# Kernel tuning notes

Hardware: AMD Instinct MI355X
Metric: run time of the kernel (lower is better)

Reference implementation:

```python
import jax, jax.numpy as jnp
import numpy as np

B, V, D, E, F, H, HD = 16, 1024, 16, 64, 16, 128, 64
GRAPH_LAYERS, FLOW_ITERS, DUAL_ITERS = 2, 10, 10
STEP, MOM, BIG = 0.01, 0.9, 1e9


def _build_graph():
    # circulant graph: node v's d-th out-neighbor is v + offs[d] (mod V); offsets paired (o, -o)
    offs = np.array([1, -1, 2, -2, 3, -3, 4, -4, 5, -5, 6, -6, 7, -7, 8, -8], dtype=np.int32)
    v = np.arange(V, dtype=np.int32)[:, None]
    d = np.broadcast_to(np.arange(D, dtype=np.int32)[None, :], (V, D))
    adj = ((v + offs[None, :]) % V).astype(np.int32)
    inv_adj = ((v - offs[None, :]) % V).astype(np.int32)
    in_idx = np.stack([inv_adj, d], axis=-1)    # d-th incoming edge of v == out-edge (inv_adj[v,d], slot d)
    rev_idx = np.stack([adj, d], axis=-1)       # out-edge (v,d) is the d-th incoming edge of adj[v,d]
    opp_idx = np.stack([adj, d ^ 1], axis=-1)   # opposite edge (w->v) is slot d^1 at w (paired offsets)
    bt = lambda x: jnp.asarray(np.broadcast_to(x[None], (B,) + x.shape).copy())
    return bt(adj), bt(inv_adj), bt(in_idx), bt(rev_idx), bt(opp_idx)


def setup_inputs() -> dict:
    key = jax.random.key(0)
    ks = jax.random.split(key, 16)
    adj_lst, inv_adj_lst, in_indices, rev_indices, opp_indices = _build_graph()
    rn = lambda k, shape, scale=1.0: jax.random.normal(k, shape, dtype=jnp.float32) * scale
    s = lambda fan: 1.0 / float(np.sqrt(fan))
    return {
        'demands': rn(ks[0], (B, V, 1)),
        'node_features': rn(ks[1], (B, V, F)),
        'edge_lengths': jax.random.uniform(ks[2], (B, V, D), dtype=jnp.float32),
        'norm_edge_lengths': jax.random.uniform(ks[3], (B, V, D), dtype=jnp.float32),
        'node_emb': rn(ks[4], (V, E)),
        'W_enc': rn(ks[5], (E + F, H), s(E + F)), 'b_enc': jnp.zeros((H,), jnp.float32),
        'W_gat': rn(ks[6], (H, H), s(H)), 'b_gat': jnp.zeros((H,), jnp.float32),
        'a_gat': rn(ks[7], (H,), s(H)),
        'W_gru_x': rn(ks[8], (H, 3 * H), s(H)), 'W_gru_h': rn(ks[9], (H, 3 * H), s(H)),
        'b_gru': jnp.zeros((3 * H,), jnp.float32),
        'W_dec1': rn(ks[10], (2 * H, HD), s(2 * H)), 'b_dec1': jnp.zeros((HD,), jnp.float32),
        'W_dec2': rn(ks[11], (HD, 1), s(HD)), 'b_dec2': jnp.zeros((1,), jnp.float32),
        'W_dual1': rn(ks[12], (H, HD), s(H)), 'b_dual1': jnp.zeros((HD,), jnp.float32),
        'W_dual2': rn(ks[13], (HD, 1), s(HD)), 'b_dual2': jnp.zeros((1,), jnp.float32),
        'adj_lst': adj_lst, 'inv_adj_lst': inv_adj_lst,
        'in_indices': in_indices, 'rev_indices': rev_indices, 'opp_indices': opp_indices,
        'num_nodes': jnp.full((B,), V, dtype=jnp.int32),
    }


def _gather_nodes(values, idx, valid):
    # masked_gather with set_zero=True: values (B,V,H), idx (B,V,D) -> (B,V,D,H)
    bb = jnp.arange(values.shape[0])[:, None, None]
    g = values[bb, jnp.clip(idx, 0, values.shape[1] - 1)]
    return g * valid[..., None]


def _gather_edges(x, idx):
    # gather_nd into a (B,V,D,...) tensor; idx (B,V,D,2) = (node, slot), batch implicit
    bb = jnp.arange(x.shape[0])[:, None, None]
    return x[bb, idx[..., 0], idx[..., 1]]


def _sparsemax(z):
    n = z.shape[-1]
    zs = jnp.sort(z, axis=-1)[..., ::-1]
    k = jnp.arange(1, n + 1, dtype=z.dtype)
    zc = jnp.cumsum(zs, axis=-1)
    support = (1.0 + k * zs) > zc
    kz = jnp.sum(support, axis=-1, keepdims=True)
    tau = (jnp.take_along_axis(zc, kz - 1, axis=-1) - 1.0) / kz.astype(z.dtype)
    return jnp.maximum(z - tau, 0.0)


def _forward(demands, node_features, edge_lengths, norm_edge_lengths, node_emb, W_enc, b_enc,
             W_gat, b_gat, a_gat, W_gru_x, W_gru_h, b_gru, W_dec1, b_dec1, W_dec2, b_dec2,
             W_dual1, b_dual1, W_dual2, b_dual2,
             adj_lst, inv_adj_lst, in_indices, rev_indices, opp_indices, num_nodes):
    f32 = jnp.float32
    # embedding lookup with max_norm=1
    nrm = jnp.linalg.norm(node_emb, axis=-1, keepdims=True)
    emb = node_emb / jnp.maximum(nrm, 1.0)
    emb_b = jnp.broadcast_to(emb[None], (demands.shape[0], V, E))
    node_enc = jnp.concatenate([emb_b, node_features], axis=-1) @ W_enc + b_enc   # (B,V,H)
    mask = (adj_lst == num_nodes[:, None, None]).astype(f32)                       # 1 = padded slot
    valid = 1.0 - mask
    initial = _gather_nodes(node_enc, adj_lst, valid)                              # (B,V,D,H)
    h = initial
    for _ in range(GRAPH_LAYERS):
        # DirectionalGAT: per-edge transform, masked attention over slots, directional regather
        t = jnp.tanh(h @ W_gat + b_gat)                                            # (B,V,D,H)
        logits = jnp.einsum('bvdh,h->bvd', t, a_gat) - BIG * mask
        attn = jax.nn.softmax(logits, axis=-1)
        node_msg = jnp.einsum('bvd,bvdh->bvh', attn, t)                            # (B,V,H)
        msg = _gather_nodes(node_msg, adj_lst, valid)
        x = jnp.tanh(msg + initial)
        # GRU cell, shared weights over all edge states
        gx = x @ W_gru_x + b_gru
        gh = h @ W_gru_h
        z = jax.nn.sigmoid(gx[..., :H] + gh[..., :H])
        r = jax.nn.sigmoid(gx[..., H:2 * H] + gh[..., H:2 * H])
        cand = jnp.tanh(gx[..., 2 * H:] + r * gh[..., 2 * H:])
        h = z * h + (1.0 - z) * cand
    # decoder over (encoding, encoding + opposite-edge encoding)
    comb = h + _gather_edges(h, opp_indices)
    dec_in = jnp.concatenate([h, comb], axis=-1)
    nw = (jnp.tanh(dec_in @ W_dec1 + b_dec1) @ W_dec2 + b_dec2)[..., 0]            # (B,V,D)
    # destination attention: normalize over incoming edges, map back to outgoing layout
    inv_mask = (inv_adj_lst == num_nodes[:, None, None]).astype(f32)
    in_w = _gather_edges(nw, in_indices)
    dest_attn = jax.nn.softmax(in_w - BIG * inv_mask, axis=-1)
    nw = _gather_edges(dest_attn, rev_indices)
    pred = nw - BIG * mask
    normalized = _sparsemax(pred) * valid
    # iterative proportional min-cost-flow solver
    def mcf_step(flow, _):
        inflow = jnp.sum(_gather_edges(flow, in_indices), axis=-1, keepdims=True)  # (B,V,1)
        return normalized * jax.nn.relu(inflow - demands), None
    flow, _ = jax.lax.scan(mcf_step, jnp.zeros_like(normalized), None, length=FLOW_ITERS)
    flow_cost = jnp.sum(flow * flow, axis=(1, 2))                                  # square cost fn
    # dual variables + dual flow (projected momentum gradient descent)
    node_states = jnp.sum(h, axis=2)                                               # (B,V,H)
    dual_vars = jax.nn.relu(jnp.tanh(node_states @ W_dual1 + b_dual1) @ W_dual2 + b_dual2)  # (B,V,1)
    dual = mask * dual_vars
    dual_tr = _gather_nodes(dual_vars, adj_lst, valid)[..., 0]
    dual_diff = dual_tr - dual                                                     # (B,V,D)
    def dual_step(carry, _):
        f, vel = carry
        grad = 2.0 * f + dual_diff                                                 # d/df [f^2 + dual_diff*f]
        vel = MOM * vel - STEP * grad
        f = jax.nn.relu(f + vel)
        return (f, vel), None
    (dual_flows, _), _ = jax.lax.scan(dual_step, (jnp.zeros_like(dual_diff), jnp.zeros_like(dual_diff)), None, length=DUAL_ITERS)
    dual_flows = dual_flows * valid
    dual_demand = jnp.sum(dual_vars * demands, axis=(1, 2))
    dual_cost = jnp.sum(dual_flows * dual_flows + dual_diff * dual_flows, axis=(1, 2)) - dual_demand
    return flow_cost - dual_cost                                                   # (B,) primal-dual gap loss


def reference(demands, node_features, edge_lengths, norm_edge_lengths, node_emb, W_enc, b_enc,
              W_gat, b_gat, a_gat, W_gru_x, W_gru_h, b_gru, W_dec1, b_dec1, W_dec2, b_dec2,
              W_dual1, b_dual1, W_dual2, b_dual2,
              adj_lst, inv_adj_lst, in_indices, rev_indices, opp_indices, num_nodes):
    return _forward(demands, node_features, edge_lengths, norm_edge_lengths, node_emb, W_enc, b_enc,
                    W_gat, b_gat, a_gat, W_gru_x, W_gru_h, b_gru, W_dec1, b_dec1, W_dec2, b_dec2,
                    W_dual1, b_dual1, W_dual2, b_dual2,
                    adj_lst, inv_adj_lst, in_indices, rev_indices, opp_indices, num_nodes)
```

## Files before the change

### kernel.cpp

```cpp
#include <hip/hip_runtime.h>
#include <hip/hip_bf16.h>

#define B 16
#define V 1024
#define D 16
#define E 64
#define F 16
#define H 128
#define HD 64
#define BV (B*V)
#define BVD (B*V*D)

#define OFF_HNB      0
#define OFF_NORM     (OFF_HNB + BV*H/2)
#define OFF_DV       (OFF_NORM + BVD)
#define OFF_WT       (OFF_DV + BV)
#define OFF_WTG      (OFF_WT + 65536)
#define OFF_WPQ      (OFF_WTG + 8192)
#define OFF_WU1T     (OFF_WPQ + 8192)
#define OFF_WENCT    (OFF_WU1T + 4096)

typedef __attribute__((ext_vector_type(8))) short bf16x8;
typedef __attribute__((ext_vector_type(4))) float f32x4;

__device__ __forceinline__ short f2bf(float f){
  __hip_bfloat16 b = __float2bfloat16(f);
  return *reinterpret_cast<short*>(&b);
}
__device__ __forceinline__ float bf2f(short s){
  __hip_bfloat16 b; *reinterpret_cast<short*>(&b) = s;
  return __bfloat162float(b);
}
__device__ __forceinline__ float frcp(float x){ return __builtin_amdgcn_rcpf(x); }
__device__ __forceinline__ float fsig(float x){ return frcp(1.f + __expf(-x)); }
__device__ __forceinline__ float ftanh(float x){
  float e = __expf(-2.f*fabsf(x));
  float r = (1.f - e)*frcp(1.f + e);
  return copysignf(r, x);
}

__global__ __launch_bounds__(256) void k_pre(const float* __restrict__ Wx, const float* __restrict__ Wh,
    const float* __restrict__ Wg, const float* __restrict__ W1, const float* __restrict__ Wu1,
    const float* __restrict__ Wenc,
    short* __restrict__ Wt, short* __restrict__ Wgt, short* __restrict__ Wpq,
    short* __restrict__ Wu1t, short* __restrict__ Wenct, float* __restrict__ outz){
  int bid = blockIdx.x, tid = threadIdx.x;
  if (bid == 0 && tid < 16) outz[tid] = 0.f;
  if (bid < 512){
    int n = bid, k = tid;
    int g = n >> 7, j = n & 127;
    float v;
    if (g == 0)      v = (k < 128) ? Wx[k*384 + j]       : Wh[(k-128)*384 + j];
    else if (g == 1) v = (k < 128) ? Wx[k*384 + 128 + j] : Wh[(k-128)*384 + 128 + j];
    else if (g == 2) v = (k < 128) ? Wx[k*384 + 256 + j] : 0.f;
    else             v = (k < 128) ? 0.f                 : Wh[(k-128)*384 + 256 + j];
    Wt[n*256 + k] = f2bf(v);
    return;
  }
  if (bid < 576){
    int idx = (bid-512)*256 + tid;
    int n = idx >> 7, k = idx & 127;
    Wgt[n*128 + k] = f2bf(Wg[k*128 + n]);
    return;
  }
  if (bid < 608){
    int idx = (bid-576)*256 + tid;
    int n = idx >> 7, k = idx & 127;
    float wb = W1[(k+128)*HD + n];
    float wa = W1[k*HD + n];
    Wpq[n*128 + k]      = f2bf(wa + wb);
    Wpq[(64+n)*128 + k] = f2bf(wb);
    return;
  }
  if (bid < 640){
    int idx = (bid-608)*256 + tid;
    int n = idx >> 7, k = idx & 127;
    Wu1t[n*128 + k] = f2bf(Wu1[k*HD + n]);
    return;
  }
  {
    int nn = (bid-640)*2 + (tid >> 7);
    int kk = tid & 127;
    if (kk < 96) Wenct[nn*96 + kk] = f2bf(kk < 80 ? Wenc[kk*128 + nn] : 0.f);
  }
}

__global__ __launch_bounds__(512,4) void k_mega(const float* __restrict__ emb, const float* __restrict__ nf,
    const short* __restrict__ Wenct, const float* __restrict__ benc, const int* __restrict__ adj,
    const short* __restrict__ Wgt, const float* __restrict__ bg, const float* __restrict__ ag,
    const short* __restrict__ Wt, const float* __restrict__ bgru, short* __restrict__ hout){
  __shared__ short NE[64][136];
  __shared__ short T[64][136];
  __shared__ short H1[48][136];
  __shared__ short X[48][136];
  __shared__ float Lp[8][64];
  __shared__ float Ls[64];
  __shared__ float nrmv[64];
  short (*As)[136] = T;

  int tid = threadIdx.x;
  int blk = blockIdx.x;
  int b = blk >> 5;
  int n0 = (blk & 31) << 5;
  int w = tid >> 6, lane = tid & 63;
  int l15 = lane & 15, quad = lane >> 4;

  if (tid < 64){
    int v = (n0 - 16 + tid) & 1023;
    const float4* e4 = reinterpret_cast<const float4*>(&emb[v*E]);
    float ss = 0.f;
    #pragma unroll
    for (int q=0;q<16;q++){ float4 x = e4[q]; ss += x.x*x.x + x.y*x.y + x.z*x.z + x.w*x.w; }
    nrmv[tid] = frcp(fmaxf(sqrtf(ss), 1.f));
  }
  __syncthreads();
  for (int e=tid; e<64*16; e+=512){
    int r = e >> 4, q = e & 15;
    int v = (n0 - 16 + r) & 1023;
    float4 x = reinterpret_cast<const float4*>(&emb[v*E])[q];
    float iv = nrmv[r];
    short4 s; s.x=f2bf(x.x*iv); s.y=f2bf(x.y*iv); s.z=f2bf(x.z*iv); s.w=f2bf(x.w*iv);
    *reinterpret_cast<short4*>(&As[r][q*4]) = s;
  }
  for (int e=tid; e<64*4; e+=512){
    int r = e >> 2, q = e & 3;
    int m = (b<<10) + ((n0 - 16 + r) & 1023);
    float4 x = reinterpret_cast<const float4*>(&nf[(long)m*F])[q];
    short4 s; s.x=f2bf(x.x); s.y=f2bf(x.y); s.z=f2bf(x.z); s.w=f2bf(x.w);
    *reinterpret_cast<short4*>(&As[r][64 + q*4]) = s;
    short4 z; z.x=0; z.y=0; z.z=0; z.w=0;
    *reinterpret_cast<short4*>(&As[r][80 + q*4]) = z;
  }
  __syncthreads();
  {
    f32x4 acc[4];
    #pragma unroll
    for (int mt=0;mt<4;mt++) acc[mt] = (f32x4){0.f,0.f,0.f,0.f};
    #pragma unroll
    for (int kc=0;kc<3;kc++){
      int k0 = kc*32;
      bf16x8 bfr = *reinterpret_cast<const bf16x8*>(&Wenct[(16*w + l15)*96 + k0 + quad*8]);
      #pragma unroll
      for (int mt=0;mt<4;mt++){
        bf16x8 a = *reinterpret_cast<const bf16x8*>(&As[16*mt + l15][k0 + quad*8]);
        acc[mt] = __builtin_amdgcn_mfma_f32_16x16x32_bf16(a, bfr, acc[mt], 0,0,0);
      }
    }
    int c = 16*w + l15;
    float bb = benc[c];
    #pragma unroll
    for (int mt=0;mt<4;mt++)
      #pragma unroll
      for (int reg=0;reg<4;reg++)
        NE[16*mt + quad*4 + reg][c] = f2bf(acc[mt][reg] + bb);
  }
  __syncthreads();
  {
    f32x4 acc[4];
    #pragma unroll
    for (int mt=0;mt<4;mt++) acc[mt] = (f32x4){0.f,0.f,0.f,0.f};
    #pragma unroll
    for (int kc=0;kc<4;kc++){
      int k0 = kc*32;
      bf16x8 bfr = *reinterpret_cast<const bf16x8*>(&Wgt[(16*w + l15)*128 + k0 + quad*8]);
      #pragma unroll
      for (int mt=0;mt<4;mt++){
        bf16x8 a = *reinterpret_cast<const bf16x8*>(&NE[16*mt + l15][k0 + quad*8]);
        acc[mt] = __builtin_amdgcn_mfma_f32_16x16x32_bf16(a, bfr, acc[mt], 0,0,0);
      }
    }
    int c = 16*w + l15;
    float bgc = bg[c], agc = ag[c];
    float lp[4][4];
    #pragma unroll
    for (int mt=0;mt<4;mt++)
      #pragma unroll
      for (int reg=0;reg<4;reg++){
        float t = ftanh(acc[mt][reg] + bgc);
        T[16*mt + quad*4 + reg][c] = f2bf(t);
        lp[mt][reg] = t * agc;
      }
    #pragma unroll
    for (int mt=0;mt<4;mt++)
      #pragma unroll
      for (int reg=0;reg<4;reg++){
        lp[mt][reg] += __shfl_xor(lp[mt][reg], 1);
        lp[mt][reg] += __shfl_xor(lp[mt][reg], 2);
        lp[mt][reg] += __shfl_xor(lp[mt][reg], 4);
        lp[mt][reg] += __shfl_xor(lp[mt][reg], 8);
      }
    if (l15 == 0){
      #pragma unroll
      for (int mt=0;mt<4;mt++)
        #pragma unroll
        for (int reg=0;reg<4;reg++)
          Lp[w][16*mt + quad*4 + reg] = lp[mt][reg];
    }
  }
  __syncthreads();
  if (tid < 64){
    float s = 0.f;
    #pragma unroll
    for (int i=0;i<8;i++) s += Lp[i][tid];
    Ls[tid] = s;
  }
  __syncthreads();
  if (tid < 192){
    int vl = tid >> 2, seg = tid & 3;
    int wg = (b<<10) + ((n0 - 8 + vl) & 1023);
    int li[16]; float at[16];
    float m = -1e30f;
    #pragma unroll
    for (int d=0; d<16; d++){
      int a = adj[wg*16 + d];
      li[d] = (a - n0 + 16) & 1023;
      m = fmaxf(m, Ls[li[d]]);
    }
    float s = 0.f;
    #pragma unroll
    for (int d=0; d<16; d++){ at[d] = __expf(Ls[li[d]] - m); s += at[d]; }
    float inv = frcp(s);
    #pragma unroll
    for (int d=0; d<16; d++) at[d] *= inv;
    #pragma unroll
    for (int c8=0; c8<4; c8++){
      int c = seg*32 + c8*8;
      float acc8[8] = {0,0,0,0,0,0,0,0};
      #pragma unroll 4
      for (int d=0; d<16; d++){
        bf16x8 tv = *reinterpret_cast<const bf16x8*>(&T[li[d]][c]);
        float a = at[d];
        #pragma unroll
        for (int q=0;q<8;q++) acc8[q] += a * bf2f(tv[q]);
      }
      bf16x8 nv = *reinterpret_cast<const bf16x8*>(&NE[vl + 8][c]);
      bf16x8 xv;
      #pragma unroll
      for (int q=0;q<8;q++) xv[q] = f2bf(ftanh(acc8[q] + bf2f(nv[q])));
      *reinterpret_cast<bf16x8*>(&X[vl][c]) = xv;
    }
  }
  __syncthreads();
  {
    f32x4 acc[3][4];
    #pragma unroll
    for (int mt=0;mt<3;mt++)
      #pragma unroll
      for (int g=0;g<4;g++) acc[mt][g] = (f32x4){0.f,0.f,0.f,0.f};
    for (int k8=0;k8<8;k8++){
      int k0 = k8*32;
      int gg = (k8 < 4) ? 2 : 3;
      int ncol = 16*w + l15;
      int koff = k0 + quad*8;
      bf16x8 bz = *reinterpret_cast<const bf16x8*>(&Wt[(ncol      )*256 + koff]);
      bf16x8 br = *reinterpret_cast<const bf16x8*>(&Wt[(ncol + 128)*256 + koff]);
      bf16x8 bc = *reinterpret_cast<const bf16x8*>(&Wt[(ncol + gg*128)*256 + koff]);
      #pragma unroll
      for (int mt=0;mt<3;mt++){
        bf16x8 a;
        if (k8 < 4) a = *reinterpret_cast<const bf16x8*>(&X[16*mt + l15][k0 + quad*8]);
        else        a = *reinterpret_cast<const bf16x8*>(&NE[16*mt + l15 + 8][k0 - 128 + quad*8]);
        acc[mt][0]  = __builtin_amdgcn_mfma_f32_16x16x32_bf16(a, bz, acc[mt][0], 0,0,0);
        acc[mt][1]  = __builtin_amdgcn_mfma_f32_16x16x32_bf16(a, br, acc[mt][1], 0,0,0);
        acc[mt][gg] = __builtin_amdgcn_mfma_f32_16x16x32_bf16(a, bc, acc[mt][gg], 0,0,0);
      }
    }
    int j = 16*w + l15;
    float bjz = bgru[j], bjr = bgru[128 + j], bjc = bgru[256 + j];
    #pragma unroll
    for (int mt=0;mt<3;mt++){
      #pragma unroll
      for (int reg=0;reg<4;reg++){
        int rl = 16*mt + quad*4 + reg;
        float z = fsig(acc[mt][0][reg] + bjz);
        float r = fsig(acc[mt][1][reg] + bjr);
        float cand = ftanh(acc[mt][2][reg] + bjc + r*acc[mt][3][reg]);
        float ho = bf2f(NE[rl + 8][j]);
        H1[rl][j] = f2bf(z*ho + (1.f - z)*cand);
      }
    }
  }
  __syncthreads();
  {
    f32x4 acc[3];
    #pragma unroll
    for (int mt=0;mt<3;mt++) acc[mt] = (f32x4){0.f,0.f,0.f,0.f};
    #pragma unroll
    for (int kc=0;kc<4;kc++){
      int k0 = kc*32;
      bf16x8 bfr = *reinterpret_cast<const bf16x8*>(&Wgt[(16*w + l15)*128 + k0 + quad*8]);
      #pragma unroll
      for (int mt=0;mt<3;mt++){
        bf16x8 a = *reinterpret_cast<const bf16x8*>(&H1[16*mt + l15][k0 + quad*8]);
        acc[mt] = __builtin_amdgcn_mfma_f32_16x16x32_bf16(a, bfr, acc[mt], 0,0,0);
      }
    }
    int c = 16*w + l15;
    float bgc = bg[c], agc = ag[c];
    float lp[3][4];
    #pragma unroll
    for (int mt=0;mt<3;mt++)
      #pragma unroll
      for (int reg=0;reg<4;reg++){
        float t = ftanh(acc[mt][reg] + bgc);
        T[16*mt + quad*4 + reg][c] = f2bf(t);
        lp[mt][reg] = t * agc;
      }
    #pragma unroll
    for (int mt=0;mt<3;mt++)
      #pragma unroll
      for (int reg=0;reg<4;reg++){
        lp[mt][reg] += __shfl_xor(lp[mt][reg], 1);
        lp[mt][reg] += __shfl_xor(lp[mt][reg], 2);
        lp[mt][reg] += __shfl_xor(lp[mt][reg], 4);
        lp[mt][reg] += __shfl_xor(lp[mt][reg], 8);
      }
    if (l15 == 0){
      #pragma unroll
      for (int mt=0;mt<3;mt++)
        #pragma unroll
        for (int reg=0;reg<4;reg++)
          Lp[w][16*mt + quad*4 + reg] = lp[mt][reg];
    }
  }
  __syncthreads();
  if (tid < 48){
    float s = 0.f;
    #pragma unroll
    for (int i=0;i<8;i++) s += Lp[i][tid];
    Ls[tid] = s;
  }
  __syncthreads();
  if (tid < 128){
    int vl = tid >> 2, seg = tid & 3;
    int vg = (b<<10) + n0 + vl;
    int li[16]; float at[16];
    float m = -1e30f;
    #pragma unroll
    for (int d=0; d<16; d++){
      int a = adj[vg*16 + d];
      li[d] = (a - n0 + 8) & 1023;
      m = fmaxf(m, Ls[li[d]]);
    }
    float s = 0.f;
    #pragma unroll
    for (int d=0; d<16; d++){ at[d] = __expf(Ls[li[d]] - m); s += at[d]; }
    float inv = frcp(s);
    #pragma unroll
    for (int d=0; d<16; d++) at[d] *= inv;
    #pragma unroll
    for (int c8=0; c8<4; c8++){
      int c = seg*32 + c8*8;
      float acc8[8] = {0,0,0,0,0,0,0,0};
      #pragma unroll 4
      for (int d=0; d<16; d++){
        bf16x8 tv = *reinterpret_cast<const bf16x8*>(&T[li[d]][c]);
        float a = at[d];
        #pragma unroll
        for (int q=0;q<8;q++) acc8[q] += a * bf2f(tv[q]);
      }
      bf16x8 nv = *reinterpret_cast<const bf16x8*>(&NE[vl + 16][c]);
      bf16x8 xv;
      #pragma unroll
      for (int q=0;q<8;q++) xv[q] = f2bf(ftanh(acc8[q] + bf2f(nv[q])));
      *reinterpret_cast<bf16x8*>(&X[vl][c]) = xv;
    }
  }
  __syncthreads();
  {
    f32x4 acc[2][4];
    #pragma unroll
    for (int mt=0;mt<2;mt++)
      #pragma unroll
      for (int g=0;g<4;g++) acc[mt][g] = (f32x4){0.f,0.f,0.f,0.f};
    for (int k8=0;k8<8;k8++){
      int k0 = k8*32;
      int gg = (k8 < 4) ? 2 : 3;
      int ncol = 16*w + l15;
      int koff = k0 + quad*8;
      bf16x8 bz = *reinterpret_cast<const bf16x8*>(&Wt[(ncol      )*256 + koff]);
      bf16x8 br = *reinterpret_cast<const bf16x8*>(&Wt[(ncol + 128)*256 + koff]);
      bf16x8 bc = *reinterpret_cast<const bf16x8*>(&Wt[(ncol + gg*128)*256 + koff]);
      #pragma unroll
      for (int mt=0;mt<2;mt++){
        bf16x8 a;
        if (k8 < 4) a = *reinterpret_cast<const bf16x8*>(&X[16*mt + l15][k0 + quad*8]);
        else        a = *reinterpret_cast<const bf16x8*>(&H1[16*mt + l15 + 8][k0 - 128 + quad*8]);
        acc[mt][0]  = __builtin_amdgcn_mfma_f32_16x16x32_bf16(a, bz, acc[mt][0], 0,0,0);
        acc[mt][1]  = __builtin_amdgcn_mfma_f32_16x16x32_bf16(a, br, acc[mt][1], 0,0,0);
        acc[mt][gg] = __builtin_amdgcn_mfma_f32_16x16x32_bf16(a, bc, acc[mt][gg], 0,0,0);
      }
    }
    __syncthreads();
    int j = 16*w + l15;
    float bjz = bgru[j], bjr = bgru[128 + j], bjc = bgru[256 + j];
    #pragma unroll
    for (int mt=0;mt<2;mt++){
      #pragma unroll
      for (int reg=0;reg<4;reg++){
        int rl = 16*mt + quad*4 + reg;
        float z = fsig(acc[mt][0][reg] + bjz);
        float r = fsig(acc[mt][1][reg] + bjr);
        float cand = ftanh(acc[mt][2][reg] + bjc + r*acc[mt][3][reg]);
        float ho = bf2f(H1[rl + 8][j]);
        X[rl][j] = f2bf(z*ho + (1.f - z)*cand);
      }
    }
  }
  __syncthreads();
  for (int idx=tid; idx<32*16; idx+=512){
    int r = idx >> 4, c8 = idx & 15;
    *reinterpret_cast<bf16x8*>(&hout[(long)((b<<10) + n0 + r)*128 + c8*8]) =
        *reinterpret_cast<const bf16x8*>(&X[r][c8*8]);
  }
}

__global__ __launch_bounds__(512,2) void k_decdas(const short* __restrict__ hn, const int* __restrict__ adj,
    const int* __restrict__ invadj, const short* __restrict__ Wpq, const float* __restrict__ b1,
    const float* __restrict__ W2, const float* __restrict__ b2_,
    const short* __restrict__ Wu1t, const float* __restrict__ bu1, const float* __restrict__ Wu2,
    const float* __restrict__ bu2_, float* __restrict__ norm_, float* __restrict__ dv){
  __shared__ short Hs[112][136];
  __shared__ short PQb[112][132];
  __shared__ short NSs[64][136];
  __shared__ int adjL[64][16];
  __shared__ float dvp[64][4];
  __shared__ float b1s[64], w2s[64], bu1s[64], wu2s[64];
  int tid = threadIdx.x;
  int blk = blockIdx.x;
  int b = blk >> 4;
  int n0 = (blk & 15) << 6;
  if (tid < 64){ b1s[tid] = b1[tid]; w2s[tid] = W2[tid]; bu1s[tid] = bu1[tid]; wu2s[tid] = Wu2[tid]; }
  for (int idx=tid; idx<112*16; idx+=512){
    int r = idx >> 4, c8 = idx & 15;
    int g = (b << 10) + ((n0 - 24 + r) & 1023);
    *reinterpret_cast<bf16x8*>(&Hs[r][c8*8]) =
        *reinterpret_cast<const bf16x8*>(&hn[(long)g*128 + c8*8]);
  }
  for (int idx=tid; idx<1024; idx+=512){
    int r = idx >> 4, d = idx & 15;
    int a = adj[((b<<10) + n0 + r)*16 + d];
    adjL[r][d] = (a - n0 + 24) & 1023;
  }
  __syncthreads();
  int w = tid >> 6, lane = tid & 63;
  int l15 = lane & 15, quad = lane >> 4;
  {
    f32x4 acc[7];
    #pragma unroll
    for (int mt=0;mt<7;mt++) acc[mt] = (f32x4){0.f,0.f,0.f,0.f};
    #pragma unroll
    for (int kc=0;kc<4;kc++){
      int k0 = kc*32;
      bf16x8 bfr = *reinterpret_cast<const bf16x8*>(&Wpq[(16*w + l15)*128 + k0 + quad*8]);
      #pragma unroll
      for (int mt=0;mt<7;mt++){
        bf16x8 a = *reinterpret_cast<const bf16x8*>(&Hs[16*mt + l15][k0 + quad*8]);
        acc[mt] = __builtin_amdgcn_mfma_f32_16x16x32_bf16(a, bfr, acc[mt], 0,0,0);
      }
    }
    int c = 16*w + l15;
    #pragma unroll
    for (int mt=0;mt<7;mt++)
      #pragma unroll
      for (int reg=0;reg<4;reg++)
        PQb[16*mt + quad*4 + reg][c] = f2bf(acc[mt][reg]);
  }
  for (int idx=tid; idx<64*16; idx+=512){
    int r = idx >> 4, c8 = idx & 15;
    float acc8[8] = {0,0,0,0,0,0,0,0};
    #pragma unroll 4
    for (int d=0; d<16; d++){
      bf16x8 hv = *reinterpret_cast<const bf16x8*>(&Hs[adjL[r][d]][c8*8]);
      #pragma unroll
      for (int q=0;q<8;q++) acc8[q] += bf2f(hv[q]);
    }
    bf16x8 sv;
    #pragma unroll
    for (int q=0;q<8;q++) sv[q] = f2bf(acc8[q]);
    *reinterpret_cast<bf16x8*>(&NSs[r][c8*8]) = sv;
  }
  __syncthreads();
  if (w < 4){
    f32x4 acc[4];
    #pragma unroll
    for (int mt=0;mt<4;mt++) acc[mt] = (f32x4){0.f,0.f,0.f,0.f};
    #pragma unroll
    for (int kc=0;kc<4;kc++){
      int k0 = kc*32;
      bf16x8 bfr = *reinterpret_cast<const bf16x8*>(&Wu1t[(16*w + l15)*128 + k0 + quad*8]);
      #pragma unroll
      for (int mt=0;mt<4;mt++){
        bf16x8 a = *reinterpret_cast<const bf16x8*>(&NSs[16*mt + l15][k0 + quad*8]);
        acc[mt] = __builtin_amdgcn_mfma_f32_16x16x32_bf16(a, bfr, acc[mt], 0,0,0);
      }
    }
    int n = 16*w + l15;
    float bn = bu1s[n], wn = wu2s[n];
    #pragma unroll
    for (int mt=0;mt<4;mt++){
      #pragma unroll
      for (int reg=0;reg<4;reg++){
        float p = ftanh(acc[mt][reg] + bn) * wn;
        p += __shfl_xor(p, 1);
        p += __shfl_xor(p, 2);
        p += __shfl_xor(p, 4);
        p += __shfl_xor(p, 8);
        if (l15 == 0) dvp[16*mt + quad*4 + reg][w] = p;
      }
    }
  }
  __syncthreads();
  float* nws = reinterpret_cast<float*>(&Hs[0][0]);
  float b2v = b2_[0];
  for (int e = tid; e < 96*16; e += 512){
    int rr = e >> 4, d = e & 15;
    int wnode = (n0 + rr - 16) & 1023;
    int wg = (b<<10) + wnode;
    int a = adj[wg*16 + d];
    int al = (a - n0 + 24) & 1023;
    int wl = rr + 8;
    float p = 0.f;
    #pragma unroll 8
    for (int c=0;c<64;c++)
      p += ftanh(bf2f(PQb[al][c]) + bf2f(PQb[wl][64 + c]) + b1s[c]) * w2s[c];
    nws[rr*17 + d] = p + b2v;
  }
  __syncthreads();
  if (tid < 64){
    float val = dvp[tid][0]+dvp[tid][1]+dvp[tid][2]+dvp[tid][3];
    dv[(b<<10) + n0 + tid] = fmaxf(val + bu2_[0], 0.f);
  }
  float* datt = reinterpret_cast<float*>(&PQb[0][0]);
  if (tid < 80){
    int wnode = (n0 + tid - 8) & 1023;
    int wg = (b<<10) + wnode;
    float vals[16];
    float m = -1e30f;
    #pragma unroll
    for (int d=0; d<16; d++){
      int iv = invadj[wg*16 + d];
      int il = (iv - n0 + 16) & 1023;
      vals[d] = nws[il*17 + d];
      m = fmaxf(m, vals[d]);
    }
    float s = 0.f;
    #pragma unroll
    for (int d=0; d<16; d++){ vals[d] = __expf(vals[d]-m); s += vals[d]; }
    float inv = frcp(s);
    #pragma unroll
    for (int d=0; d<16; d++) datt[tid*17 + d] = vals[d]*inv;
  }
  __syncthreads();
  if (tid < 64){
    int vg = (b<<10) + n0 + tid;
    float z[16], s[16];
    #pragma unroll
    for (int d=0; d<16; d++){
      int al = adjL[tid][d] - 16;
      z[d] = datt[al*17 + d];
      s[d] = z[d];
    }
    #pragma unroll
    for (int k2 = 2; k2 <= 16; k2 <<= 1){
      #pragma unroll
      for (int jj = k2 >> 1; jj > 0; jj >>= 1){
        #pragma unroll
        for (int i = 0; i < 16; i++){
          int l = i ^ jj;
          if (l > i){
            bool up = ((i & k2) == 0);
            float a = s[i], bb = s[l];
            bool sw = up ? (a > bb) : (a < bb);
            if (sw){ s[i]=bb; s[l]=a; }
          }
        }
      }
    }
    float cs = 0.f, zcs = 0.f; int kz = 1;
    #pragma unroll
    for (int j=0;j<16;j++){
      float zj = s[15-j];
      cs += zj;
      if (1.f + (float)(j+1)*zj > cs){ kz = j+1; zcs = cs; }
    }
    float tau = (zcs - 1.f)/(float)kz;
    #pragma unroll
    for (int d=0; d<16; d++) norm_[(long)vg*16 + d] = fmaxf(z[d]-tau, 0.f);
  }
}

__global__ __launch_bounds__(256) void k_flowfin(const float* __restrict__ norm_,
    const float* __restrict__ dem, const int* __restrict__ invadj, const float* __restrict__ dv,
    float* __restrict__ out){
  __shared__ float nrmS[224*17];
  __shared__ float sbuf[2][224];
  __shared__ float red[4];
  int tid = threadIdx.x;
  int blk = blockIdx.x;
  int b = blk >> 4;
  int t0 = (blk & 15) << 6;
  for (int e=tid; e<224*4; e+=256){
    int r = e >> 2, q4 = e & 3;
    int v = (t0 - 80 + r) & 1023;
    float4 x = reinterpret_cast<const float4*>(&norm_[(long)((b<<10) + v)*16])[q4];
    nrmS[r*17 + q4*4+0] = x.x; nrmS[r*17 + q4*4+1] = x.y;
    nrmS[r*17 + q4*4+2] = x.z; nrmS[r*17 + q4*4+3] = x.w;
  }
  bool act = tid < 224;
  int r = tid;
  float dm = 0.f; int gv = 0;
  int ivl[16];
  if (act){
    int v = (t0 - 80 + r) & 1023;
    gv = (b<<10) + v;
    dm = dem[gv];
    #pragma unroll
    for (int d4=0; d4<4; d4++){
      int4 i4 = reinterpret_cast<const int4*>(&invadj[(long)gv*16])[d4];
      int t;
      t = (i4.x - t0 + 80) & 1023; ivl[d4*4+0] = t < 224 ? t : 223;
      t = (i4.y - t0 + 80) & 1023; ivl[d4*4+1] = t < 224 ? t : 223;
      t = (i4.z - t0 + 80) & 1023; ivl[d4*4+2] = t < 224 ? t : 223;
      t = (i4.w - t0 + 80) & 1023; ivl[d4*4+3] = t < 224 ? t : 223;
    }
    sbuf[0][r] = 0.f;
  }
  __syncthreads();
  float nrg[16];
  if (act){
    #pragma unroll
    for (int d=0; d<16; d++) nrg[d] = nrmS[ivl[d]*17 + d];
  }
  int p = 0;
  float s = 0.f;
  for (int it=0; it<10; it++){
    if (act){
      float inflow = 0.f;
      #pragma unroll
      for (int d=0; d<16; d++) inflow += nrg[d]*sbuf[p][ivl[d]];
      s = fmaxf(inflow - dm, 0.f);
      sbuf[1-p][r] = s;
    }
    p ^= 1;
    __syncthreads();
  }
  float partF = 0.f, partD = 0.f, partDD = 0.f;
  if (act && r >= 80 && r < 144){
    float nr2 = 0.f;
    #pragma unroll
    for (int d=0; d<16; d++){ float nv = nrmS[r*17 + d]; nr2 += nv*nv; }
    partF = nr2 * s * s;
    float dvv = dv[gv];
    float f = 0.f, vel = 0.f;
    #pragma unroll
    for (int it=0; it<10; it++){
      float g = 2.f*f + dvv;
      vel = 0.9f*vel - 0.01f*g;
      f = fmaxf(f + vel, 0.f);
    }
    partD = f*f + dvv*f;
    partDD = dvv * dm;
  }
  float val = partF - 16.f*partD + partDD;
  #pragma unroll
  for (int off=32; off>0; off>>=1) val += __shfl_down(val, off);
  if ((tid & 63) == 0) red[tid>>6] = val;
  __syncthreads();
  if (tid == 0) atomicAdd(&out[b], red[0]+red[1]+red[2]+red[3]);
}

extern "C" void kernel_launch(void* const* d_in, const int* in_sizes, int n_in,
                              void* d_out, int out_size, void* d_ws, size_t ws_size,
                              hipStream_t stream){
  (void)in_sizes; (void)n_in; (void)out_size; (void)ws_size;
  const float* demands = (const float*)d_in[0];
  const float* nf      = (const float*)d_in[1];
  const float* emb     = (const float*)d_in[4];
  const float* Wenc    = (const float*)d_in[5];
  const float* benc    = (const float*)d_in[6];
  const float* Wgat    = (const float*)d_in[7];
  const float* bgat    = (const float*)d_in[8];
  const float* agat    = (const float*)d_in[9];
  const float* Wgx     = (const float*)d_in[10];
  const float* Wgh     = (const float*)d_in[11];
  const float* bgru    = (const float*)d_in[12];
  const float* Wd1     = (const float*)d_in[13];
  const float* bd1     = (const float*)d_in[14];
  const float* Wd2     = (const float*)d_in[15];
  const float* bd2     = (const float*)d_in[16];
  const float* Wu1     = (const float*)d_in[17];
  const float* bu1     = (const float*)d_in[18];
  const float* Wu2     = (const float*)d_in[19];
  const float* bu2     = (const float*)d_in[20];
  const int* adj       = (const int*)d_in[21];
  const int* invadj    = (const int*)d_in[22];

  float* ws    = (float*)d_ws;
  short* hnB   = (short*)(ws + OFF_HNB);
  float* nrm   = ws + OFF_NORM;
  float* dv    = ws + OFF_DV;
  short* wt    = (short*)(ws + OFF_WT);
  short* wtg   = (short*)(ws + OFF_WTG);
  short* wpq   = (short*)(ws + OFF_WPQ);
  short* wu1t  = (short*)(ws + OFF_WU1T);
  short* wenct = (short*)(ws + OFF_WENCT);

  k_pre<<<704, 256, 0, stream>>>(Wgx, Wgh, Wgat, Wd1, Wu1, Wenc, wt, wtg, wpq, wu1t, wenct,
                                 (float*)d_out);
  k_mega<<<BV/32, 512, 0, stream>>>(emb, nf, wenct, benc, adj, wtg, bgat, agat, wt, bgru, hnB);
  k_decdas<<<BV/64, 512, 0, stream>>>(hnB, adj, invadj, wpq, bd1, Wd2, bd2,
                                      wu1t, bu1, Wu2, bu2, nrm, dv);
  k_flowfin<<<B*16, 256, 0, stream>>>(nrm, demands, invadj, dv, (float*)d_out);
}
```

Measured before the change: 194.4 us.

## Widen graph tiles to 64 nodes, GAT aggregation as dense MFMA, 1024-thread decoder

k_mega now processes 64 output nodes per block instead of 32, cutting the halo recomputation of the encoder/GAT/GRU layers relative to useful rows. The attention-weighted neighbor aggregation is rewritten as a dense banded attention matrix (A2) times a transposed T tile on MFMA instead of scalar gather-FMA loops. Adjacency is loaded once per thread and reused for both layers. k_decdas is relaunched with 1024 threads, splitting its MFMA and neighbor-sum work across more waves. The trade-off is more LDS per block, lower occupancy bounds, and extra zero-fill of the mostly sparse A2 matrix.

```diff
diff --git a/kernel.cpp b/kernel.cpp
--- a/kernel.cpp
+++ b/kernel.cpp
@@ -85,36 +85,54 @@
   }
 }
 
-__global__ __launch_bounds__(512,4) void k_mega(const float* __restrict__ emb, const float* __restrict__ nf,
+__global__ __launch_bounds__(512,2) void k_mega(const float* __restrict__ emb, const float* __restrict__ nf,
     const short* __restrict__ Wenct, const float* __restrict__ benc, const int* __restrict__ adj,
     const short* __restrict__ Wgt, const float* __restrict__ bg, const float* __restrict__ ag,
     const short* __restrict__ Wt, const float* __restrict__ bgru, short* __restrict__ hout){
-  __shared__ short NE[64][136];
-  __shared__ short T[64][136];
-  __shared__ short H1[48][136];
-  __shared__ short X[48][136];
-  __shared__ float Lp[8][64];
-  __shared__ float Ls[64];
-  __shared__ float nrmv[64];
-  short (*As)[136] = T;
+  __shared__ short NE[96][136];
+  __shared__ short Tt[128][104];
+  __shared__ short H1[80][136];
+  __shared__ short X[80][136];
+  __shared__ short A2[80][104];
+  __shared__ float Lp[8][96];
+  __shared__ float Ls[96];
+  __shared__ float nrmv[96];
+  short (*As)[104] = reinterpret_cast<short(*)[104]>(&H1[0][0]);
 
   int tid = threadIdx.x;
   int blk = blockIdx.x;
-  int b = blk >> 5;
-  int n0 = (blk & 31) << 5;
+  int b = blk >> 4;
+  int n0 = (blk & 15) << 6;
   int w = tid >> 6, lane = tid & 63;
   int l15 = lane & 15, quad = lane >> 4;
 
-  if (tid < 64){
-    int v = (n0 - 16 + tid) & 1023;
+  int li96[16];
+  if (tid < 80){
+    int wg = (b<<10) + ((n0 - 8 + tid) & 1023);
+    const int4* a4 = reinterpret_cast<const int4*>(&adj[(long)wg*16]);
+    #pragma unroll
+    for (int d4=0; d4<4; d4++){
+      int4 i4 = a4[d4];
+      li96[d4*4+0] = (i4.x - n0 + 16) & 1023;
+      li96[d4*4+1] = (i4.y - n0 + 16) & 1023;
+      li96[d4*4+2] = (i4.z - n0 + 16) & 1023;
+      li96[d4*4+3] = (i4.w - n0 + 16) & 1023;
+    }
+  }
+
+  if (tid < 384){
+    int r = tid >> 2, q = tid & 3;
+    int v = (n0 - 16 + r) & 1023;
     const float4* e4 = reinterpret_cast<const float4*>(&emb[v*E]);
     float ss = 0.f;
     #pragma unroll
-    for (int q=0;q<16;q++){ float4 x = e4[q]; ss += x.x*x.x + x.y*x.y + x.z*x.z + x.w*x.w; }
-    nrmv[tid] = frcp(fmaxf(sqrtf(ss), 1.f));
-  }
-  __syncthreads();
-  for (int e=tid; e<64*16; e+=512){
+    for (int qq=0;qq<4;qq++){ float4 x = e4[q*4+qq]; ss += x.x*x.x + x.y*x.y + x.z*x.z + x.w*x.w; }
+    ss += __shfl_xor(ss, 1);
+    ss += __shfl_xor(ss, 2);
+    if (q == 0) nrmv[r] = frcp(fmaxf(sqrtf(ss), 1.f));
+  }
+  __syncthreads();
+  for (int e=tid; e<96*16; e+=512){
     int r = e >> 4, q = e & 15;
     int v = (n0 - 16 + r) & 1023;
     float4 x = reinterpret_cast<const float4*>(&emb[v*E])[q];
@@ -122,7 +140,7 @@
     short4 s; s.x=f2bf(x.x*iv); s.y=f2bf(x.y*iv); s.z=f2bf(x.z*iv); s.w=f2bf(x.w*iv);
     *reinterpret_cast<short4*>(&As[r][q*4]) = s;
   }
-  for (int e=tid; e<64*4; e+=512){
+  for (int e=tid; e<96*4; e+=512){
     int r = e >> 2, q = e & 3;
     int m = (b<<10) + ((n0 - 16 + r) & 1023);
     float4 x = reinterpret_cast<const float4*>(&nf[(long)m*F])[q];
@@ -133,15 +151,15 @@
   }
   __syncthreads();
   {
-    f32x4 acc[4];
-    #pragma unroll
-    for (int mt=0;mt<4;mt++) acc[mt] = (f32x4){0.f,0.f,0.f,0.f};
+    f32x4 acc[6];
+    #pragma unroll
+    for (int mt=0;mt<6;mt++) acc[mt] = (f32x4){0.f,0.f,0.f,0.f};
     #pragma unroll
     for (int kc=0;kc<3;kc++){
       int k0 = kc*32;
       bf16x8 bfr = *reinterpret_cast<const bf16x8*>(&Wenct[(16*w + l15)*96 + k0 + quad*8]);
       #pragma unroll
-      for (int mt=0;mt<4;mt++){
+      for (int mt=0;mt<6;mt++){
         bf16x8 a = *reinterpret_cast<const bf16x8*>(&As[16*mt + l15][k0 + quad*8]);
         acc[mt] = __builtin_amdgcn_mfma_f32_16x16x32_bf16(a, bfr, acc[mt], 0,0,0);
       }
@@ -149,39 +167,42 @@
     int c = 16*w + l15;
     float bb = benc[c];
     #pragma unroll
-    for (int mt=0;mt<4;mt++)
+    for (int mt=0;mt<6;mt++)
       #pragma unroll
       for (int reg=0;reg<4;reg++)
         NE[16*mt + quad*4 + reg][c] = f2bf(acc[mt][reg] + bb);
   }
   __syncthreads();
   {
-    f32x4 acc[4];
-    #pragma unroll
-    for (int mt=0;mt<4;mt++) acc[mt] = (f32x4){0.f,0.f,0.f,0.f};
+    f32x4 acc[6];
+    #pragma unroll
+    for (int mt=0;mt<6;mt++) acc[mt] = (f32x4){0.f,0.f,0.f,0.f};
     #pragma unroll
     for (int kc=0;kc<4;kc++){
       int k0 = kc*32;
       bf16x8 bfr = *reinterpret_cast<const bf16x8*>(&Wgt[(16*w + l15)*128 + k0 + quad*8]);
       #pragma unroll
-      for (int mt=0;mt<4;mt++){
+      for (int mt=0;mt<6;mt++){
         bf16x8 a = *reinterpret_cast<const bf16x8*>(&NE[16*mt + l15][k0 + quad*8]);
         acc[mt] = __builtin_amdgcn_mfma_f32_16x16x32_bf16(a, bfr, acc[mt], 0,0,0);
       }
     }
     int c = 16*w + l15;
     float bgc = bg[c], agc = ag[c];
-    float lp[4][4];
-    #pragma unroll
-    for (int mt=0;mt<4;mt++)
+    float lp[6][4];
+    #pragma unroll
+    for (int mt=0;mt<6;mt++){
+      short4 tv;
       #pragma unroll
       for (int reg=0;reg<4;reg++){
         float t = ftanh(acc[mt][reg] + bgc);
-        T[16*mt + quad*4 + reg][c] = f2bf(t);
+        reinterpret_cast<short*>(&tv)[reg] = f2bf(t);
         lp[mt][reg] = t * agc;
       }
-    #pragma unroll
-    for (int mt=0;mt<4;mt++)
+      *reinterpret_cast<short4*>(&Tt[c][16*mt + quad*4]) = tv;
+    }
+    #pragma unroll
+    for (int mt=0;mt<6;mt++)
       #pragma unroll
       for (int reg=0;reg<4;reg++){
         lp[mt][reg] += __shfl_xor(lp[mt][reg], 1);
@@ -191,60 +212,70 @@
       }
     if (l15 == 0){
       #pragma unroll
-      for (int mt=0;mt<4;mt++)
+      for (int mt=0;mt<6;mt++)
         #pragma unroll
         for (int reg=0;reg<4;reg++)
           Lp[w][16*mt + quad*4 + reg] = lp[mt][reg];
     }
   }
   __syncthreads();
-  if (tid < 64){
+  if (tid < 96){
     float s = 0.f;
     #pragma unroll
     for (int i=0;i<8;i++) s += Lp[i][tid];
     Ls[tid] = s;
   }
-  __syncthreads();
-  if (tid < 192){
-    int vl = tid >> 2, seg = tid & 3;
-    int wg = (b<<10) + ((n0 - 8 + vl) & 1023);
-    int li[16]; float at[16];
+  {
+    bf16x8 z8;
+    #pragma unroll
+    for (int q=0;q<8;q++) z8[q] = 0;
+    for (int idx=tid; idx<960; idx+=512){
+      int r = idx/12, c8 = idx%12;
+      *reinterpret_cast<bf16x8*>(&A2[r][c8*8]) = z8;
+    }
+  }
+  __syncthreads();
+  if (tid < 80){
+    float at[16];
     float m = -1e30f;
     #pragma unroll
-    for (int d=0; d<16; d++){
-      int a = adj[wg*16 + d];
-      li[d] = (a - n0 + 16) & 1023;
-      m = fmaxf(m, Ls[li[d]]);
-    }
+    for (int d=0; d<16; d++) m = fmaxf(m, Ls[li96[d]]);
     float s = 0.f;
     #pragma unroll
-    for (int d=0; d<16; d++){ at[d] = __expf(Ls[li[d]] - m); s += at[d]; }
+    for (int d=0; d<16; d++){ at[d] = __expf(Ls[li96[d]] - m); s += at[d]; }
     float inv = frcp(s);
     #pragma unroll
-    for (int d=0; d<16; d++) at[d] *= inv;
-    #pragma unroll
-    for (int c8=0; c8<4; c8++){
-      int c = seg*32 + c8*8;
-      float acc8[8] = {0,0,0,0,0,0,0,0};
-      #pragma unroll 4
-      for (int d=0; d<16; d++){
-        bf16x8 tv = *reinterpret_cast<const bf16x8*>(&T[li[d]][c]);
-        float a = at[d];
-        #pragma unroll
-        for (int q=0;q<8;q++) acc8[q] += a * bf2f(tv[q]);
-      }
-      bf16x8 nv = *reinterpret_cast<const bf16x8*>(&NE[vl + 8][c]);
-      bf16x8 xv;
-      #pragma unroll
-      for (int q=0;q<8;q++) xv[q] = f2bf(ftanh(acc8[q] + bf2f(nv[q])));
-      *reinterpret_cast<bf16x8*>(&X[vl][c]) = xv;
-    }
-  }
-  __syncthreads();
-  {
-    f32x4 acc[3][4];
-    #pragma unroll
-    for (int mt=0;mt<3;mt++)
+    for (int d=0; d<16; d++) A2[tid][li96[d]] = f2bf(at[d]*inv);
+  }
+  __syncthreads();
+  {
+    f32x4 acc[5];
+    #pragma unroll
+    for (int mt=0;mt<5;mt++) acc[mt] = (f32x4){0.f,0.f,0.f,0.f};
+    #pragma unroll
+    for (int kc=0;kc<3;kc++){
+      int k0 = kc*32;
+      bf16x8 bfr = *reinterpret_cast<const bf16x8*>(&Tt[16*w + l15][k0 + quad*8]);
+      #pragma unroll
+      for (int mt=0;mt<5;mt++){
+        bf16x8 a = *reinterpret_cast<const bf16x8*>(&A2[16*mt + l15][k0 + quad*8]);
+        acc[mt] = __builtin_amdgcn_mfma_f32_16x16x32_bf16(a, bfr, acc[mt], 0,0,0);
+      }
+    }
+    int c = 16*w + l15;
+    #pragma unroll
+    for (int mt=0;mt<5;mt++)
+      #pragma unroll
+      for (int reg=0;reg<4;reg++){
+        int rl = 16*mt + quad*4 + reg;
+        X[rl][c] = f2bf(ftanh(acc[mt][reg] + bf2f(NE[rl + 8][c])));
+      }
+  }
+  __syncthreads();
+  {
+    f32x4 acc[5][4];
+    #pragma unroll
+    for (int mt=0;mt<5;mt++)
       #pragma unroll
       for (int g=0;g<4;g++) acc[mt][g] = (f32x4){0.f,0.f,0.f,0.f};
     for (int k8=0;k8<8;k8++){
@@ -256,7 +287,7 @@
       bf16x8 br = *reinterpret_cast<const bf16x8*>(&Wt[(ncol + 128)*256 + koff]);
       bf16x8 bc = *reinterpret_cast<const bf16x8*>(&Wt[(ncol + gg*128)*256 + koff]);
       #pragma unroll
-      for (int mt=0;mt<3;mt++){
+      for (int mt=0;mt<5;mt++){
         bf16x8 a;
         if (k8 < 4) a = *reinterpret_cast<const bf16x8*>(&X[16*mt + l15][k0 + quad*8]);
         else        a = *reinterpret_cast<const bf16x8*>(&NE[16*mt + l15 + 8][k0 - 128 + quad*8]);
@@ -268,7 +299,7 @@
     int j = 16*w + l15;
     float bjz = bgru[j], bjr = bgru[128 + j], bjc = bgru[256 + j];
     #pragma unroll
-    for (int mt=0;mt<3;mt++){
+    for (int mt=0;mt<5;mt++){
       #pragma unroll
       for (int reg=0;reg<4;reg++){
         int rl = 16*mt + quad*4 + reg;
@@ -282,32 +313,35 @@
   }
   __syncthreads();
   {
-    f32x4 acc[3];
-    #pragma unroll
-    for (int mt=0;mt<3;mt++) acc[mt] = (f32x4){0.f,0.f,0.f,0.f};
+    f32x4 acc[5];
+    #pragma unroll
+    for (int mt=0;mt<5;mt++) acc[mt] = (f32x4){0.f,0.f,0.f,0.f};
     #pragma unroll
     for (int kc=0;kc<4;kc++){
       int k0 = kc*32;
       bf16x8 bfr = *reinterpret_cast<const bf16x8*>(&Wgt[(16*w + l15)*128 + k0 + quad*8]);
       #pragma unroll
-      for (int mt=0;mt<3;mt++){
+      for (int mt=0;mt<5;mt++){
         bf16x8 a = *reinterpret_cast<const bf16x8*>(&H1[16*mt + l15][k0 + quad*8]);
         acc[mt] = __builtin_amdgcn_mfma_f32_16x16x32_bf16(a, bfr, acc[mt], 0,0,0);
       }
     }
     int c = 16*w + l15;
     float bgc = bg[c], agc = ag[c];
-    float lp[3][4];
-    #pragma unroll
-    for (int mt=0;mt<3;mt++)
+    float lp[5][4];
+    #pragma unroll
+    for (int mt=0;mt<5;mt++){
+      short4 tv;
       #pragma unroll
       for (int reg=0;reg<4;reg++){
         float t = ftanh(acc[mt][reg] + bgc);
-        T[16*mt + quad*4 + reg][c] = f2bf(t);
+        reinterpret_cast<short*>(&tv)[reg] = f2bf(t);
         lp[mt][reg] = t * agc;
       }
-    #pragma unroll
-    for (int mt=0;mt<3;mt++)
+      *reinterpret_cast<short4*>(&Tt[c][16*mt + quad*4]) = tv;
+    }
+    #pragma unroll
+    for (int mt=0;mt<5;mt++)
       #pragma unroll
       for (int reg=0;reg<4;reg++){
         lp[mt][reg] += __shfl_xor(lp[mt][reg], 1);
@@ -317,60 +351,71 @@
       }
     if (l15 == 0){
       #pragma unroll
-      for (int mt=0;mt<3;mt++)
+      for (int mt=0;mt<5;mt++)
         #pragma unroll
         for (int reg=0;reg<4;reg++)
           Lp[w][16*mt + quad*4 + reg] = lp[mt][reg];
     }
   }
   __syncthreads();
-  if (tid < 48){
+  if (tid < 80){
     float s = 0.f;
     #pragma unroll
     for (int i=0;i<8;i++) s += Lp[i][tid];
     Ls[tid] = s;
   }
-  __syncthreads();
-  if (tid < 128){
-    int vl = tid >> 2, seg = tid & 3;
-    int vg = (b<<10) + n0 + vl;
-    int li[16]; float at[16];
+  {
+    bf16x8 z8;
+    #pragma unroll
+    for (int q=0;q<8;q++) z8[q] = 0;
+    for (int idx=tid; idx<768; idx+=512){
+      int r = idx/12, c8 = idx%12;
+      *reinterpret_cast<bf16x8*>(&A2[r][c8*8]) = z8;
+    }
+  }
+  __syncthreads();
+  if (tid >= 8 && tid < 72){
+    int r5 = tid - 8;
+    float at[16];
     float m = -1e30f;
     #pragma unroll
-    for (int d=0; d<16; d++){
-      int a = adj[vg*16 + d];
-      li[d] = (a - n0 + 8) & 1023;
-      m = fmaxf(m, Ls[li[d]]);
-    }
+    for (int d=0; d<16; d++) m = fmaxf(m, Ls[li96[d] - 8]);
     float s = 0.f;
     #pragma unroll
-    for (int d=0; d<16; d++){ at[d] = __expf(Ls[li[d]] - m); s += at[d]; }
+    for (int d=0; d<16; d++){ at[d] = __expf(Ls[li96[d] - 8] - m); s += at[d]; }
     float inv = frcp(s);
     #pragma unroll
-    for (int d=0; d<16; d++) at[d] *= inv;
-    #pragma unroll
-    for (int c8=0; c8<4; c8++){
-      int c = seg*32 + c8*8;
-      float acc8[8] = {0,0,0,0,0,0,0,0};
-      #pragma unroll 4
-      for (int d=0; d<16; d++){
-        bf16x8 tv = *reinterpret_cast<const bf16x8*>(&T[li[d]][c]);
-        float a = at[d];
-        #pragma unroll
-        for (int q=0;q<8;q++) acc8[q] += a * bf2f(tv[q]);
-      }
-      bf16x8 nv = *reinterpret_cast<const bf16x8*>(&NE[vl + 16][c]);
-      bf16x8 xv;
-      #pragma unroll
-      for (int q=0;q<8;q++) xv[q] = f2bf(ftanh(acc8[q] + bf2f(nv[q])));
-      *reinterpret_cast<bf16x8*>(&X[vl][c]) = xv;
-    }
-  }
-  __syncthreads();
-  {
-    f32x4 acc[2][4];
-    #pragma unroll
-    for (int mt=0;mt<2;mt++)
+    for (int d=0; d<16; d++) A2[r5][li96[d] - 8] = f2bf(at[d]*inv);
+  }
+  __syncthreads();
+  {
+    f32x4 acc[4];
+    #pragma unroll
+    for (int mt=0;mt<4;mt++) acc[mt] = (f32x4){0.f,0.f,0.f,0.f};
+    #pragma unroll
+    for (int kc=0;kc<3;kc++){
+      int k0 = kc*32;
+      bf16x8 bfr = *reinterpret_cast<const bf16x8*>(&Tt[16*w + l15][k0 + quad*8]);
+      #pragma unroll
+      for (int mt=0;mt<4;mt++){
+        bf16x8 a = *reinterpret_cast<const bf16x8*>(&A2[16*mt + l15][k0 + quad*8]);
+        acc[mt] = __builtin_amdgcn_mfma_f32_16x16x32_bf16(a, bfr, acc[mt], 0,0,0);
+      }
+    }
+    int c = 16*w + l15;
+    #pragma unroll
+    for (int mt=0;mt<4;mt++)
+      #pragma unroll
+      for (int reg=0;reg<4;reg++){
+        int rl = 16*mt + quad*4 + reg;
+        X[rl][c] = f2bf(ftanh(acc[mt][reg] + bf2f(NE[rl + 16][c])));
+      }
+  }
+  __syncthreads();
+  {
+    f32x4 acc[4][4];
+    #pragma unroll
+    for (int mt=0;mt<4;mt++)
       #pragma unroll
       for (int g=0;g<4;g++) acc[mt][g] = (f32x4){0.f,0.f,0.f,0.f};
     for (int k8=0;k8<8;k8++){
@@ -382,7 +427,7 @@
       bf16x8 br = *reinterpret_cast<const bf16x8*>(&Wt[(ncol + 128)*256 + koff]);
       bf16x8 bc = *reinterpret_cast<const bf16x8*>(&Wt[(ncol + gg*128)*256 + koff]);
       #pragma unroll
-      for (int mt=0;mt<2;mt++){
+      for (int mt=0;mt<4;mt++){
         bf16x8 a;
         if (k8 < 4) a = *reinterpret_cast<const bf16x8*>(&X[16*mt + l15][k0 + quad*8]);
         else        a = *reinterpret_cast<const bf16x8*>(&H1[16*mt + l15 + 8][k0 - 128 + quad*8]);
@@ -395,7 +440,7 @@
     int j = 16*w + l15;
     float bjz = bgru[j], bjr = bgru[128 + j], bjc = bgru[256 + j];
     #pragma unroll
-    for (int mt=0;mt<2;mt++){
+    for (int mt=0;mt<4;mt++){
       #pragma unroll
       for (int reg=0;reg<4;reg++){
         int rl = 16*mt + quad*4 + reg;
@@ -408,14 +453,14 @@
     }
   }
   __syncthreads();
-  for (int idx=tid; idx<32*16; idx+=512){
+  for (int idx=tid; idx<64*16; idx+=512){
     int r = idx >> 4, c8 = idx & 15;
     *reinterpret_cast<bf16x8*>(&hout[(long)((b<<10) + n0 + r)*128 + c8*8]) =
         *reinterpret_cast<const bf16x8*>(&X[r][c8*8]);
   }
 }
 
-__global__ __launch_bounds__(512,2) void k_decdas(const short* __restrict__ hn, const int* __restrict__ adj,
+__global__ __launch_bounds__(1024,4) void k_decdas(const short* __restrict__ hn, const int* __restrict__ adj,
     const int* __restrict__ invadj, const short* __restrict__ Wpq, const float* __restrict__ b1,
     const float* __restrict__ W2, const float* __restrict__ b2_,
     const short* __restrict__ Wu1t, const float* __restrict__ bu1, const float* __restrict__ Wu2,
@@ -431,43 +476,51 @@
   int b = blk >> 4;
   int n0 = (blk & 15) << 6;
   if (tid < 64){ b1s[tid] = b1[tid]; w2s[tid] = W2[tid]; bu1s[tid] = bu1[tid]; wu2s[tid] = Wu2[tid]; }
-  for (int idx=tid; idx<112*16; idx+=512){
+  for (int idx=tid; idx<112*16; idx+=1024){
     int r = idx >> 4, c8 = idx & 15;
     int g = (b << 10) + ((n0 - 24 + r) & 1023);
     *reinterpret_cast<bf16x8*>(&Hs[r][c8*8]) =
         *reinterpret_cast<const bf16x8*>(&hn[(long)g*128 + c8*8]);
   }
-  for (int idx=tid; idx<1024; idx+=512){
-    int r = idx >> 4, d = idx & 15;
+  {
+    int r = tid >> 4, d = tid & 15;
     int a = adj[((b<<10) + n0 + r)*16 + d];
     adjL[r][d] = (a - n0 + 24) & 1023;
   }
   __syncthreads();
   int w = tid >> 6, lane = tid & 63;
   int l15 = lane & 15, quad = lane >> 4;
-  {
-    f32x4 acc[7];
-    #pragma unroll
-    for (int mt=0;mt<7;mt++) acc[mt] = (f32x4){0.f,0.f,0.f,0.f};
+  int cw = w & 7, hw = w >> 3;
+  {
+    f32x4 acc[4];
+    #pragma unroll
+    for (int t=0;t<4;t++) acc[t] = (f32x4){0.f,0.f,0.f,0.f};
     #pragma unroll
     for (int kc=0;kc<4;kc++){
       int k0 = kc*32;
-      bf16x8 bfr = *reinterpret_cast<const bf16x8*>(&Wpq[(16*w + l15)*128 + k0 + quad*8]);
-      #pragma unroll
-      for (int mt=0;mt<7;mt++){
-        bf16x8 a = *reinterpret_cast<const bf16x8*>(&Hs[16*mt + l15][k0 + quad*8]);
-        acc[mt] = __builtin_amdgcn_mfma_f32_16x16x32_bf16(a, bfr, acc[mt], 0,0,0);
-      }
-    }
-    int c = 16*w + l15;
-    #pragma unroll
-    for (int mt=0;mt<7;mt++)
-      #pragma unroll
-      for (int reg=0;reg<4;reg++)
-        PQb[16*mt + quad*4 + reg][c] = f2bf(acc[mt][reg]);
-  }
-  for (int idx=tid; idx<64*16; idx+=512){
-    int r = idx >> 4, c8 = idx & 15;
+      bf16x8 bfr = *reinterpret_cast<const bf16x8*>(&Wpq[(16*cw + l15)*128 + k0 + quad*8]);
+      #pragma unroll
+      for (int t=0;t<4;t++){
+        int mt = 4*hw + t;
+        if (mt < 7){
+          bf16x8 a = *reinterpret_cast<const bf16x8*>(&Hs[16*mt + l15][k0 + quad*8]);
+          acc[t] = __builtin_amdgcn_mfma_f32_16x16x32_bf16(a, bfr, acc[t], 0,0,0);
+        }
+      }
+    }
+    int c = 16*cw + l15;
+    #pragma unroll
+    for (int t=0;t<4;t++){
+      int mt = 4*hw + t;
+      if (mt < 7){
+        #pragma unroll
+        for (int reg=0;reg<4;reg++)
+          PQb[16*mt + quad*4 + reg][c] = f2bf(acc[t][reg]);
+      }
+    }
+  }
+  {
+    int r = tid >> 4, c8 = tid & 15;
     float acc8[8] = {0,0,0,0,0,0,0,0};
     #pragma unroll 4
     for (int d=0; d<16; d++){
@@ -481,39 +534,40 @@
     *reinterpret_cast<bf16x8*>(&NSs[r][c8*8]) = sv;
   }
   __syncthreads();
-  if (w < 4){
-    f32x4 acc[4];
-    #pragma unroll
-    for (int mt=0;mt<4;mt++) acc[mt] = (f32x4){0.f,0.f,0.f,0.f};
+  if (w < 8){
+    int c4 = w & 3, h2 = w >> 2;
+    f32x4 acc[2];
+    #pragma unroll
+    for (int t=0;t<2;t++) acc[t] = (f32x4){0.f,0.f,0.f,0.f};
     #pragma unroll
     for (int kc=0;kc<4;kc++){
       int k0 = kc*32;
-      bf16x8 bfr = *reinterpret_cast<const bf16x8*>(&Wu1t[(16*w + l15)*128 + k0 + quad*8]);
-      #pragma unroll
-      for (int mt=0;mt<4;mt++){
-        bf16x8 a = *reinterpret_cast<const bf16x8*>(&NSs[16*mt + l15][k0 + quad*8]);
-        acc[mt] = __builtin_amdgcn_mfma_f32_16x16x32_bf16(a, bfr, acc[mt], 0,0,0);
-      }
-    }
-    int n = 16*w + l15;
+      bf16x8 bfr = *reinterpret_cast<const bf16x8*>(&Wu1t[(16*c4 + l15)*128 + k0 + quad*8]);
+      #pragma unroll
+      for (int t=0;t<2;t++){
+        bf16x8 a = *reinterpret_cast<const bf16x8*>(&NSs[16*(2*h2+t) + l15][k0 + quad*8]);
+        acc[t] = __builtin_amdgcn_mfma_f32_16x16x32_bf16(a, bfr, acc[t], 0,0,0);
+      }
+    }
+    int n = 16*c4 + l15;
     float bn = bu1s[n], wn = wu2s[n];
     #pragma unroll
-    for (int mt=0;mt<4;mt++){
-      #pragma unroll
-      for (int reg=0;reg<4;reg++){
-        float p = ftanh(acc[mt][reg] + bn) * wn;
+    for (int t=0;t<2;t++){
+      #pragma unroll
+      for (int reg=0;reg<4;reg++){
+        float p = ftanh(acc[t][reg] + bn) * wn;
         p += __shfl_xor(p, 1);
         p += __shfl_xor(p, 2);
         p += __shfl_xor(p, 4);
         p += __shfl_xor(p, 8);
-        if (l15 == 0) dvp[16*mt + quad*4 + reg][w] = p;
+        if (l15 == 0) dvp[16*(2*h2+t) + quad*4 + reg][c4] = p;
       }
     }
   }
   __syncthreads();
   float* nws = reinterpret_cast<float*>(&Hs[0][0]);
   float b2v = b2_[0];
-  for (int e = tid; e < 96*16; e += 512){
+  for (int e = tid; e < 96*16; e += 1024){
     int rr = e >> 4, d = e & 15;
     int wnode = (n0 + rr - 16) & 1023;
     int wg = (b<<10) + wnode;
@@ -708,8 +762,8 @@
 
   k_pre<<<704, 256, 0, stream>>>(Wgx, Wgh, Wgat, Wd1, Wu1, Wenc, wt, wtg, wpq, wu1t, wenct,
                                  (float*)d_out);
-  k_mega<<<BV/32, 512, 0, stream>>>(emb, nf, wenct, benc, adj, wtg, bgat, agat, wt, bgru, hnB);
-  k_decdas<<<BV/64, 512, 0, stream>>>(hnB, adj, invadj, wpq, bd1, Wd2, bd2,
-                                      wu1t, bu1, Wu2, bu2, nrm, dv);
+  k_mega<<<BV/64, 512, 0, stream>>>(emb, nf, wenct, benc, adj, wtg, bgat, agat, wt, bgru, hnB);
+  k_decdas<<<BV/64, 1024, 0, stream>>>(hnB, adj, invadj, wpq, bd1, Wd2, bd2,
+                                       wu1t, bu1, Wu2, bu2, nrm, dv);
   k_flowfin<<<B*16, 256, 0, stream>>>(nrm, demands, invadj, dv, (float*)d_out);
 }
```

Result: faster. 176.6 us (-9.2%).
